# Kernel tuning notes

Hardware: AMD Instinct MI355X
Metric: run time of the kernel (lower is better)

Reference implementation:

```python
import jax, jax.numpy as jnp
import numpy as np

N, F, H, C = 50000, 128, 4, 32   # nodes, in_channels, heads, hidden_channels
E, R, DE = 800000, 8, 64         # edges, num_relations, edge_dim


def setup_inputs() -> dict:
    key = jax.random.key(0)
    ks = jax.random.split(key, 10)
    x = jax.random.normal(ks[0], (N, F), dtype=jnp.float32)
    edge_index = jax.random.randint(ks[1], (2, E), 0, N, dtype=jnp.int64)
    edge_type = jax.random.randint(ks[2], (E,), 0, R, dtype=jnp.int64)
    s_in = 1.0 / np.sqrt(F)
    s_e = 1.0 / np.sqrt(DE)
    edge_emb = jax.random.normal(ks[3], (R, DE), dtype=jnp.float32)
    Wq = jax.random.normal(ks[4], (F, H * C), dtype=jnp.float32) * s_in
    Wk = jax.random.normal(ks[5], (F, H * C), dtype=jnp.float32) * s_in
    Wv = jax.random.normal(ks[6], (F, H * C), dtype=jnp.float32) * s_in
    We = jax.random.normal(ks[7], (DE, H * C), dtype=jnp.float32) * s_e
    Wskip = jax.random.normal(ks[8], (F, H * C), dtype=jnp.float32) * s_in
    return {"x": x, "edge_index": edge_index, "edge_type": edge_type,
            "edge_emb": edge_emb, "Wq": Wq, "Wk": Wk, "Wv": Wv,
            "We": We, "Wskip": Wskip}


def reference(x, edge_index, edge_type, edge_emb, Wq, Wk, Wv, We, Wskip):
    # TransformerConv (PyG) with edge embeddings, concat heads, root skip, no bias.
    src, dst = edge_index[0], edge_index[1]
    q = (x @ Wq).reshape(N, H, C)
    k = (x @ Wk).reshape(N, H, C)
    v = (x @ Wv).reshape(N, H, C)
    e = (edge_emb[edge_type] @ We).reshape(E, H, C)      # per-edge relation emb
    kj = k[src] + e                                       # [E,H,C]
    logits = (q[dst] * kj).sum(-1) / jnp.sqrt(jnp.float32(C))  # [E,H]
    # segment softmax over incoming edges of each target node
    m = jax.ops.segment_max(logits, dst, num_segments=N)  # [N,H]
    m = jnp.where(jnp.isfinite(m), m, jnp.float32(0.0))
    ex = jnp.exp(logits - m[dst])
    denom = jax.ops.segment_sum(ex, dst, num_segments=N)  # [N,H]
    alpha = ex / (denom[dst] + 1e-16)                     # [E,H]
    msg = (v[src] + e) * alpha[:, :, None]                # [E,H,C]
    out = jax.ops.segment_sum(msg, dst, num_segments=N).reshape(N, H * C)
    return out + x @ Wskip
```

## Files before the change

kernel.cpp:

```cpp
#include <hip/hip_runtime.h>
#include <hip/hip_bf16.h>

#define NN 50000
#define FF 128
#define NH 4
#define CH 32
#define HC 128
#define NE 800000
#define NR 8
#define DEDIM 64
#define NBLK 196
#define PBLK 782
#define QKB 625
#define MTILES 3125

typedef __hip_bfloat16 bf16;
typedef __attribute__((ext_vector_type(8))) short short8;
typedef __attribute__((ext_vector_type(4))) float f32x4;

__device__ __forceinline__ float bflo(unsigned u) { return __uint_as_float(u << 16); }
__device__ __forceinline__ float bfhi(unsigned u) { return __uint_as_float(u & 0xFFFF0000u); }

__device__ __forceinline__ unsigned short f2bf(float f) {
  unsigned u = __float_as_uint(f);
  unsigned r = (u + 0x7FFFu + ((u >> 16) & 1u)) >> 16;
  return (unsigned short)r;
}
__device__ __forceinline__ unsigned pack2bf(float lo, float hi) {
  return (unsigned)f2bf(lo) | ((unsigned)f2bf(hi) << 16);
}

template <int ISBF>
__device__ __forceinline__ float ldf(const void* p, size_t i) {
  if (ISBF) return __bfloat162float(((const bf16*)p)[i]);
  return ((const float*)p)[i];
}

__global__ __launch_bounds__(256) void k_wt(const unsigned* __restrict__ xw,
    const void* __restrict__ Wq, const void* __restrict__ Ws,
    const void* __restrict__ Wk, const void* __restrict__ Wv,
    unsigned short* __restrict__ wtr) {
  unsigned ex = (xw[threadIdx.x & 63] >> 7) & 0xFFu;
  unsigned long long bb = __ballot(ex < 90u || ex > 140u);
  int isbf = (bb == 0ULL);
  int i = blockIdx.x * 256 + threadIdx.x;
  int m = i >> 14, n = (i >> 7) & 127, k = i & 127;
  const void* W = (m == 0) ? Wq : (m == 1) ? Ws : (m == 2) ? Wk : Wv;
  wtr[i] = isbf ? ((const unsigned short*)W)[k * HC + n]
                : f2bf(((const float*)W)[k * HC + n]);
}

__global__ __launch_bounds__(256) void k_prep(const unsigned* __restrict__ xw,
    const int* __restrict__ eidx32, const void* __restrict__ etype,
    const void* __restrict__ emb, const void* __restrict__ We,
    int* __restrict__ flag, int* __restrict__ hist, float* __restrict__ ee,
    unsigned* __restrict__ drk, int* __restrict__ setp) {
  __shared__ float es[NR * DEDIM];
  __shared__ int nzIdx, badBf;
  if (blockIdx.x < PBLK) {
    unsigned long long b = __ballot(eidx32[2 * (threadIdx.x & 63) + 1] != 0);
    int is64 = (b == 0ULL);
    int e0 = (blockIdx.x * 256 + threadIdx.x) * 4;
    if (e0 >= NE) return;
    int src[4], dst[4], et[4];
    if (is64) {
      const int4* p4 = (const int4*)eidx32;
      int4 a = p4[e0 >> 1],         b2 = p4[(e0 >> 1) + 1];
      int4 c = p4[(NE + e0) >> 1],  d  = p4[((NE + e0) >> 1) + 1];
      const int4* t4 = (const int4*)etype;
      int4 t0 = t4[e0 >> 1], t1 = t4[(e0 >> 1) + 1];
      src[0] = a.x; src[1] = a.z; src[2] = b2.x; src[3] = b2.z;
      dst[0] = c.x; dst[1] = c.z; dst[2] = d.x;  dst[3] = d.z;
      et[0] = t0.x; et[1] = t0.z; et[2] = t1.x;  et[3] = t1.z;
    } else {
      const int4* p4 = (const int4*)eidx32;
      int4 a = p4[e0 >> 2];
      int4 c = p4[(NE + e0) >> 2];
      const int4* t4 = (const int4*)etype;
      int4 t0 = t4[e0 >> 2];
      src[0] = a.x; src[1] = a.y; src[2] = a.z; src[3] = a.w;
      dst[0] = c.x; dst[1] = c.y; dst[2] = c.z; dst[3] = c.w;
      et[0] = t0.x; et[1] = t0.y; et[2] = t0.z; et[3] = t0.w;
    }
    unsigned dr[4]; int sp[4];
#pragma unroll
    for (int u = 0; u < 4; ++u) {
      int s  = min(max(src[u], 0), NN - 1);
      int dd = min(max(dst[u], 0), NN - 1);
      int tt = min(max(et[u], 0), NR - 1);
      int rank = atomicAdd(&hist[dd], 1);
      dr[u] = ((unsigned)dd << 16) | ((unsigned)rank & 0xFFFFu);
      sp[u] = (s << 3) | tt;
    }
    *(uint4*)&drk[e0]  = make_uint4(dr[0], dr[1], dr[2], dr[3]);
    *(int4*)&setp[e0]  = make_int4(sp[0], sp[1], sp[2], sp[3]);
    return;
  }
  if (threadIdx.x == 0) { nzIdx = 0; badBf = 0; }
  __syncthreads();
  if (threadIdx.x < 128) {
    if (eidx32[2 * threadIdx.x + 1] != 0) atomicAdd(&nzIdx, 1);
    unsigned e = (xw[threadIdx.x] >> 7) & 0xFFu;
    if (e < 90u || e > 140u) atomicAdd(&badBf, 1);
  }
  __syncthreads();
  const int isbf = (badBf == 0);
  if (threadIdx.x == 0) { flag[0] = (nzIdx == 0); flag[1] = isbf; }
  for (int i = threadIdx.x; i < NR * DEDIM; i += 256)
    es[i] = isbf ? ldf<1>(emb, i) : ldf<0>(emb, i);
  __syncthreads();
  for (int o = threadIdx.x; o < NR * HC; o += 256) {
    int r = o >> 7, j = o & 127;
    float acc = 0.f;
    if (isbf) { for (int d = 0; d < DEDIM; ++d) acc += es[r * DEDIM + d] * ldf<1>(We, d * HC + j); }
    else      { for (int d = 0; d < DEDIM; ++d) acc += es[r * DEDIM + d] * ldf<0>(We, d * HC + j); }
    ee[o] = acc;
  }
}

template <int ISBF>
__device__ __forceinline__ void qkvs4_body(const void* __restrict__ x,
    const unsigned short* __restrict__ wtr,
    unsigned short* __restrict__ qb, unsigned* __restrict__ kvb,
    void* __restrict__ out, unsigned char* __restrict__ est) {
  const int tid  = threadIdx.x;
  const int lane = tid & 63;
  const int wv   = tid >> 6;
  const int quad = lane >> 4;
  const int lr   = lane & 15;
  short8 bf[4][2][4];
#pragma unroll
  for (int m = 0; m < 4; ++m)
#pragma unroll
    for (int t = 0; t < 2; ++t) {
      int ncol = wv * 32 + t * 16 + lr;
#pragma unroll
      for (int kb = 0; kb < 4; ++kb)
        bf[m][t][kb] = *(const short8*)&wtr[(m * HC + ncol) * FF + kb * 32 + quad * 8];
    }
  unsigned short* qs  = (unsigned short*)est;
  unsigned short* sbs = (unsigned short*)(est + 4096);
  float*          sfs = (float*)(est + 4096);
  unsigned*       kvs = (unsigned*)est;
  const unsigned short* xu = (const unsigned short*)x;
  const float* xf = (const float*)x;
  const int mc = blockIdx.x;
  short8 lda[4];
  float4 raw[8];
  {
    size_t off = (size_t)(mc * 16 + lr) * FF + quad * 8;
    if (ISBF) {
#pragma unroll
      for (int kb = 0; kb < 4; ++kb) lda[kb] = *(const short8*)(xu + off + kb * 32);
    } else {
#pragma unroll
      for (int kb = 0; kb < 4; ++kb) {
        raw[2 * kb]     = *(const float4*)(xf + off + kb * 32);
        raw[2 * kb + 1] = *(const float4*)(xf + off + kb * 32 + 4);
      }
    }
  }
  for (int mt = mc; mt < MTILES; mt += QKB) {
    int m0 = mt * 16;
    short8 cur[4];
    if (ISBF) {
#pragma unroll
      for (int kb = 0; kb < 4; ++kb) cur[kb] = lda[kb];
    } else {
#pragma unroll
      for (int kb = 0; kb < 4; ++kb) {
        float4 a = raw[2 * kb], b = raw[2 * kb + 1];
        short8 o;
        o[0] = (short)f2bf(a.x); o[1] = (short)f2bf(a.y);
        o[2] = (short)f2bf(a.z); o[3] = (short)f2bf(a.w);
        o[4] = (short)f2bf(b.x); o[5] = (short)f2bf(b.y);
        o[6] = (short)f2bf(b.z); o[7] = (short)f2bf(b.w);
        cur[kb] = o;
      }
    }
    int mtn = mt + QKB;
    if (mtn < MTILES) {
      size_t off = (size_t)(mtn * 16 + lr) * FF + quad * 8;
      if (ISBF) {
#pragma unroll
        for (int kb = 0; kb < 4; ++kb) lda[kb] = *(const short8*)(xu + off + kb * 32);
      } else {
#pragma unroll
        for (int kb = 0; kb < 4; ++kb) {
          raw[2 * kb]     = *(const float4*)(xf + off + kb * 32);
          raw[2 * kb + 1] = *(const float4*)(xf + off + kb * 32 + 4);
        }
      }
    }
    f32x4 acc[4][2];
#pragma unroll
    for (int m = 0; m < 4; ++m)
#pragma unroll
      for (int t = 0; t < 2; ++t) acc[m][t] = {0.f, 0.f, 0.f, 0.f};
#pragma unroll
    for (int kb = 0; kb < 4; ++kb)
#pragma unroll
      for (int m = 0; m < 4; ++m) {
        acc[m][0] = __builtin_amdgcn_mfma_f32_16x16x32_bf16(cur[kb], bf[m][0][kb], acc[m][0], 0, 0, 0);
        acc[m][1] = __builtin_amdgcn_mfma_f32_16x16x32_bf16(cur[kb], bf[m][1][kb], acc[m][1], 0, 0, 0);
      }
#pragma unroll
    for (int t = 0; t < 2; ++t)
#pragma unroll
      for (int r = 0; r < 4; ++r) {
        int li = (quad * 4 + r) * HC + wv * 32 + t * 16 + lr;
        qs[li] = f2bf(acc[0][t][r]);
        if (ISBF) sbs[li] = f2bf(acc[1][t][r]);
        else      sfs[li] = acc[1][t][r];
      }
    __syncthreads();
    {
      int row = tid >> 4, seg = tid & 15;
      *(uint4*)(qb + (size_t)(m0 + row) * HC + seg * 8) = ((const uint4*)qs)[tid];
      if (ISBF) {
        *(uint4*)((unsigned short*)out + (size_t)(m0 + row) * HC + seg * 8) =
            ((const uint4*)sbs)[tid];
      } else {
#pragma unroll
        for (int s = 0; s < 2; ++s) {
          int idx = s * 256 + tid, rw = idx >> 5, sg = idx & 31;
          *(uint4*)((float*)out + (size_t)(m0 + rw) * HC + sg * 4) =
              ((const uint4*)sfs)[idx];
        }
      }
    }
    __syncthreads();
#pragma unroll
    for (int t = 0; t < 2; ++t)
#pragma unroll
      for (int r = 0; r < 4; ++r) {
        int li = (quad * 4 + r) * HC + wv * 32 + t * 16 + lr;
        kvs[li] = pack2bf(acc[2][t][r], acc[3][t][r]);
      }
    __syncthreads();
#pragma unroll
    for (int s = 0; s < 2; ++s) {
      int idx = s * 256 + tid, rw = idx >> 5, sg = idx & 31;
      *(uint4*)(kvb + (size_t)(m0 + rw) * HC + sg * 4) = ((const uint4*)kvs)[idx];
    }
    __syncthreads();
  }
}

__global__ __launch_bounds__(256, 2) void k_qkvs(const unsigned* __restrict__ xw,
    const unsigned short* __restrict__ wtr,
    unsigned short* __restrict__ qb, unsigned* __restrict__ kvb,
    void* __restrict__ out) {
  __shared__ __align__(16) unsigned char est[12288];
  unsigned ex = (xw[threadIdx.x & 63] >> 7) & 0xFFu;
  unsigned long long bb = __ballot(ex < 90u || ex > 140u);
  int isbf = (bb == 0ULL);
  if (isbf) qkvs4_body<1>(xw, wtr, qb, kvb, out, est);
  else      qkvs4_body<0>(xw, wtr, qb, kvb, out, est);
}

__global__ __launch_bounds__(256) void k_scan1(const int* __restrict__ hist,
                                               int* __restrict__ bsum) {
  __shared__ int red[4];
  int i = blockIdx.x * 256 + threadIdx.x;
  int v = (i < NN) ? hist[i] : 0;
#pragma unroll
  for (int m = 1; m < 64; m <<= 1) v += __shfl_xor(v, m);
  if ((threadIdx.x & 63) == 0) red[threadIdx.x >> 6] = v;
  __syncthreads();
  if (threadIdx.x == 0) bsum[blockIdx.x] = red[0] + red[1] + red[2] + red[3];
}

__global__ __launch_bounds__(256) void k_scan13(const int* __restrict__ hist,
    const int* __restrict__ bsum, int* __restrict__ rowptr) {
  __shared__ int s[256];
  int t = threadIdx.x;
  int bv = (t < NBLK) ? bsum[t] : 0;
  s[t] = bv;
  __syncthreads();
  for (int off = 1; off < 256; off <<= 1) {
    int u = (t >= off) ? s[t - off] : 0;
    __syncthreads();
    s[t] += u;
    __syncthreads();
  }
  int bexc = (blockIdx.x == 0) ? 0 : s[blockIdx.x - 1];
  __syncthreads();
  int i = blockIdx.x * 256 + t;
  int v = (i < NN) ? hist[i] : 0;
  s[t] = v;
  __syncthreads();
  for (int off = 1; off < 256; off <<= 1) {
    int u = (t >= off) ? s[t - off] : 0;
    __syncthreads();
    s[t] += u;
    __syncthreads();
  }
  int excl = bexc + s[t] - v;
  if (i < NN) rowptr[i] = excl;
  if (i == 0) rowptr[NN] = NE;
}

__global__ __launch_bounds__(256) void k_scatter(const unsigned* __restrict__ drk,
    const int* __restrict__ setp, const int* __restrict__ rowptr,
    int* __restrict__ srcet) {
  int e0 = (blockIdx.x * 256 + threadIdx.x) * 4;
  if (e0 >= NE) return;
  uint4 d4 = *(const uint4*)&drk[e0];
  int4  s4 = *(const int4*)&setp[e0];
  unsigned dd[4] = {d4.x, d4.y, d4.z, d4.w};
  int      sp[4] = {s4.x, s4.y, s4.z, s4.w};
#pragma unroll
  for (int u = 0; u < 4; ++u) {
    int pos = rowptr[dd[u] >> 16] + (int)(dd[u] & 0xFFFFu);
    pos = min(max(pos, 0), NE - 1);
    srcet[pos] = sp[u];
  }
}

__global__ __launch_bounds__(256) void k_gather(const int* __restrict__ rowptr,
    const int* __restrict__ srcet, const unsigned short* __restrict__ qb,
    const unsigned* __restrict__ kvb, const float* __restrict__ ee,
    const int* __restrict__ flag, void* __restrict__ out) {
  int n = blockIdx.x * 4 + (threadIdx.x >> 6);
  int l = threadIdx.x & 63;
  int t = l >> 5;
  int w = l & 31;
  int j0 = ((w >> 3) << 5) + ((w & 7) << 2);
  int beg = __builtin_amdgcn_readfirstlane(rowptr[n]);
  int end = __builtin_amdgcn_readfirstlane(rowptr[n + 1]);
  uint2 qw = *(const uint2*)(qb + (size_t)n * HC + j0);
  float q0 = bflo(qw.x), q1 = bfhi(qw.x), q2 = bflo(qw.y), q3 = bfhi(qw.y);
  const float sc = 0.17677669529663687f;
  float dn = 0.f, a0 = 0.f, a1 = 0.f, a2 = 0.f, a3 = 0.f;
  int p = beg;
  for (; p + 8 <= end; p += 8) {
    int se[4]; uint4 kv[4]; float4 ev[4];
#pragma unroll
    for (int u = 0; u < 4; ++u) se[u] = srcet[p + 2 * u + t];
#pragma unroll
    for (int u = 0; u < 4; ++u)
      kv[u] = *(const uint4*)(kvb + (size_t)(se[u] >> 3) * HC + j0);
#pragma unroll
    for (int u = 0; u < 4; ++u)
      ev[u] = *(const float4*)(ee + ((se[u] & 7) << 7) + j0);
#pragma unroll
    for (int u = 0; u < 4; ++u) {
      float pp = q0 * (bflo(kv[u].x) + ev[u].x) + q1 * (bflo(kv[u].y) + ev[u].y)
               + q2 * (bflo(kv[u].z) + ev[u].z) + q3 * (bflo(kv[u].w) + ev[u].w);
      pp += __shfl_xor(pp, 1);
      pp += __shfl_xor(pp, 2);
      pp += __shfl_xor(pp, 4);
      float xx = __expf(pp * sc);
      dn += xx;
      a0 += (bfhi(kv[u].x) + ev[u].x) * xx;
      a1 += (bfhi(kv[u].y) + ev[u].y) * xx;
      a2 += (bfhi(kv[u].z) + ev[u].z) * xx;
      a3 += (bfhi(kv[u].w) + ev[u].w) * xx;
    }
  }
  if (p < end) {
    int se[4]; bool ok[4]; uint4 kv[4]; float4 ev[4];
#pragma unroll
    for (int u = 0; u < 4; ++u) {
      int pe = p + 2 * u + t;
      ok[u] = pe < end;
      se[u] = srcet[ok[u] ? pe : beg];
    }
#pragma unroll
    for (int u = 0; u < 4; ++u)
      kv[u] = *(const uint4*)(kvb + (size_t)(se[u] >> 3) * HC + j0);
#pragma unroll
    for (int u = 0; u < 4; ++u)
      ev[u] = *(const float4*)(ee + ((se[u] & 7) << 7) + j0);
#pragma unroll
    for (int u = 0; u < 4; ++u) {
      float pp = q0 * (bflo(kv[u].x) + ev[u].x) + q1 * (bflo(kv[u].y) + ev[u].y)
               + q2 * (bflo(kv[u].z) + ev[u].z) + q3 * (bflo(kv[u].w) + ev[u].w);
      pp += __shfl_xor(pp, 1);
      pp += __shfl_xor(pp, 2);
      pp += __shfl_xor(pp, 4);
      float xx = ok[u] ? __expf(pp * sc) : 0.f;
      dn += xx;
      a0 += (bfhi(kv[u].x) + ev[u].x) * xx;
      a1 += (bfhi(kv[u].y) + ev[u].y) * xx;
      a2 += (bfhi(kv[u].z) + ev[u].z) * xx;
      a3 += (bfhi(kv[u].w) + ev[u].w) * xx;
    }
  }
  dn += __shfl_xor(dn, 32);
  a0 += __shfl_xor(a0, 32);
  a1 += __shfl_xor(a1, 32);
  a2 += __shfl_xor(a2, 32);
  a3 += __shfl_xor(a3, 32);
  if (t == 0) {
    float inv = 1.f / (dn + 1e-16f);
    size_t oi = (size_t)n * HC + j0;
    if (flag[1]) {
      uint2 sk = *(const uint2*)((const unsigned short*)out + oi);
      uint2 o;
      o.x = pack2bf(a0 * inv + bflo(sk.x), a1 * inv + bfhi(sk.x));
      o.y = pack2bf(a2 * inv + bflo(sk.y), a3 * inv + bfhi(sk.y));
      *(uint2*)((unsigned short*)out + oi) = o;
    } else {
      float4 sk = *(const float4*)((const float*)out + oi);
      float4 o = make_float4(a0 * inv + sk.x, a1 * inv + sk.y,
                             a2 * inv + sk.z, a3 * inv + sk.w);
      *(float4*)((float*)out + oi) = o;
    }
  }
}

extern "C" void kernel_launch(void* const* d_in, const int* in_sizes, int n_in,
                              void* d_out, int out_size, void* d_ws, size_t ws_size,
                              hipStream_t stream) {
  const void* x     = d_in[0];
  const void* eidx  = d_in[1];
  const void* etype = d_in[2];
  const void* emb   = d_in[3];
  const void* Wq    = d_in[4];
  const void* Wk    = d_in[5];
  const void* Wv    = d_in[6];
  const void* We    = d_in[7];
  const void* Ws    = d_in[8];

  float* base   = (float*)d_ws;
  int*   flag   = (int*)base;
  float* ee     = base + 16;
  int*   rowptr = (int*)(base + 1040);
  int*   bsum   = (int*)(base + 51044);
  unsigned short* wtr = (unsigned short*)(base + 51568);
  int*   srcet  = (int*)(base + 101568);
  int*   hist   = srcet;
  unsigned* drk = (unsigned*)(base + 901568);
  int*   setp   = (int*)(base + 1701568);
  unsigned short* qb  = (unsigned short*)(base + 2501568);
  unsigned*       kvb = (unsigned*)(base + 5701568);

  hipMemsetAsync(hist, 0, NN * sizeof(int), stream);
  k_wt     <<<256, 256, 0, stream>>>((const unsigned*)x, Wq, Ws, Wk, Wv, wtr);
  k_prep   <<<PBLK + 1, 256, 0, stream>>>((const unsigned*)x, (const int*)eidx,
                                          etype, emb, We, flag, hist, ee,
                                          drk, setp);
  k_qkvs   <<<QKB, 256, 0, stream>>>((const unsigned*)x, wtr, qb, kvb, d_out);
  k_scan1  <<<NBLK, 256, 0, stream>>>(hist, bsum);
  k_scan13 <<<NBLK, 256, 0, stream>>>(hist, bsum, rowptr);
  k_scatter<<<PBLK, 256, 0, stream>>>(drk, setp, rowptr, srcet);
  k_gather <<<NN / 4, 256, 0, stream>>>(rowptr, srcet, qb, kvb, ee, flag, d_out);
}
```

Baseline: 256.0 us.

## Fuse QKV projection and edge prep kernels; zero histogram inside weight transpose

Merges the QKV/skip projection kernel and the edge preprocessing kernel into one launch, with block ranges dispatched by block index. The histogram memset moves into the weight-transpose kernel. This removes a memset and one kernel launch, and lets the compute-bound GEMM blocks overlap with the atomic-heavy edge-prep blocks. The fused kernel loses the min-occupancy launch-bounds hint of the GEMM kernel, which may change register allocation.

```diff
diff --git a/kernel.cpp b/kernel.cpp
--- a/kernel.cpp
+++ b/kernel.cpp
@@ -39,7 +39,7 @@
 __global__ __launch_bounds__(256) void k_wt(const unsigned* __restrict__ xw,
     const void* __restrict__ Wq, const void* __restrict__ Ws,
     const void* __restrict__ Wk, const void* __restrict__ Wv,
-    unsigned short* __restrict__ wtr) {
+    unsigned short* __restrict__ wtr, int* __restrict__ hist) {
   unsigned ex = (xw[threadIdx.x & 63] >> 7) & 0xFFu;
   unsigned long long bb = __ballot(ex < 90u || ex > 140u);
   int isbf = (bb == 0ULL);
@@ -48,19 +48,159 @@
   const void* W = (m == 0) ? Wq : (m == 1) ? Ws : (m == 2) ? Wk : Wv;
   wtr[i] = isbf ? ((const unsigned short*)W)[k * HC + n]
                 : f2bf(((const float*)W)[k * HC + n]);
-}
-
-__global__ __launch_bounds__(256) void k_prep(const unsigned* __restrict__ xw,
+  if (i < NN) hist[i] = 0;
+}
+
+template <int ISBF>
+__device__ __forceinline__ void qkvs4_body(const void* __restrict__ x,
+    const unsigned short* __restrict__ wtr,
+    unsigned short* __restrict__ qb, unsigned* __restrict__ kvb,
+    void* __restrict__ out, unsigned char* __restrict__ est) {
+  const int tid  = threadIdx.x;
+  const int lane = tid & 63;
+  const int wv   = tid >> 6;
+  const int quad = lane >> 4;
+  const int lr   = lane & 15;
+  short8 bf[4][2][4];
+#pragma unroll
+  for (int m = 0; m < 4; ++m)
+#pragma unroll
+    for (int t = 0; t < 2; ++t) {
+      int ncol = wv * 32 + t * 16 + lr;
+#pragma unroll
+      for (int kb = 0; kb < 4; ++kb)
+        bf[m][t][kb] = *(const short8*)&wtr[(m * HC + ncol) * FF + kb * 32 + quad * 8];
+    }
+  unsigned short* qs  = (unsigned short*)est;
+  unsigned short* sbs = (unsigned short*)(est + 4096);
+  float*          sfs = (float*)(est + 4096);
+  unsigned*       kvs = (unsigned*)est;
+  const unsigned short* xu = (const unsigned short*)x;
+  const float* xf = (const float*)x;
+  const int mc = blockIdx.x;
+  short8 lda[4];
+  float4 raw[8];
+  {
+    size_t off = (size_t)(mc * 16 + lr) * FF + quad * 8;
+    if (ISBF) {
+#pragma unroll
+      for (int kb = 0; kb < 4; ++kb) lda[kb] = *(const short8*)(xu + off + kb * 32);
+    } else {
+#pragma unroll
+      for (int kb = 0; kb < 4; ++kb) {
+        raw[2 * kb]     = *(const float4*)(xf + off + kb * 32);
+        raw[2 * kb + 1] = *(const float4*)(xf + off + kb * 32 + 4);
+      }
+    }
+  }
+  for (int mt = mc; mt < MTILES; mt += QKB) {
+    int m0 = mt * 16;
+    short8 cur[4];
+    if (ISBF) {
+#pragma unroll
+      for (int kb = 0; kb < 4; ++kb) cur[kb] = lda[kb];
+    } else {
+#pragma unroll
+      for (int kb = 0; kb < 4; ++kb) {
+        float4 a = raw[2 * kb], b = raw[2 * kb + 1];
+        short8 o;
+        o[0] = (short)f2bf(a.x); o[1] = (short)f2bf(a.y);
+        o[2] = (short)f2bf(a.z); o[3] = (short)f2bf(a.w);
+        o[4] = (short)f2bf(b.x); o[5] = (short)f2bf(b.y);
+        o[6] = (short)f2bf(b.z); o[7] = (short)f2bf(b.w);
+        cur[kb] = o;
+      }
+    }
+    int mtn = mt + QKB;
+    if (mtn < MTILES) {
+      size_t off = (size_t)(mtn * 16 + lr) * FF + quad * 8;
+      if (ISBF) {
+#pragma unroll
+        for (int kb = 0; kb < 4; ++kb) lda[kb] = *(const short8*)(xu + off + kb * 32);
+      } else {
+#pragma unroll
+        for (int kb = 0; kb < 4; ++kb) {
+          raw[2 * kb]     = *(const float4*)(xf + off + kb * 32);
+          raw[2 * kb + 1] = *(const float4*)(xf + off + kb * 32 + 4);
+        }
+      }
+    }
+    f32x4 acc[4][2];
+#pragma unroll
+    for (int m = 0; m < 4; ++m)
+#pragma unroll
+      for (int t = 0; t < 2; ++t) acc[m][t] = {0.f, 0.f, 0.f, 0.f};
+#pragma unroll
+    for (int kb = 0; kb < 4; ++kb)
+#pragma unroll
+      for (int m = 0; m < 4; ++m) {
+        acc[m][0] = __builtin_amdgcn_mfma_f32_16x16x32_bf16(cur[kb], bf[m][0][kb], acc[m][0], 0, 0, 0);
+        acc[m][1] = __builtin_amdgcn_mfma_f32_16x16x32_bf16(cur[kb], bf[m][1][kb], acc[m][1], 0, 0, 0);
+      }
+#pragma unroll
+    for (int t = 0; t < 2; ++t)
+#pragma unroll
+      for (int r = 0; r < 4; ++r) {
+        int li = (quad * 4 + r) * HC + wv * 32 + t * 16 + lr;
+        qs[li] = f2bf(acc[0][t][r]);
+        if (ISBF) sbs[li] = f2bf(acc[1][t][r]);
+        else      sfs[li] = acc[1][t][r];
+      }
+    __syncthreads();
+    {
+      int row = tid >> 4, seg = tid & 15;
+      *(uint4*)(qb + (size_t)(m0 + row) * HC + seg * 8) = ((const uint4*)qs)[tid];
+      if (ISBF) {
+        *(uint4*)((unsigned short*)out + (size_t)(m0 + row) * HC + seg * 8) =
+            ((const uint4*)sbs)[tid];
+      } else {
+#pragma unroll
+        for (int s = 0; s < 2; ++s) {
+          int idx = s * 256 + tid, rw = idx >> 5, sg = idx & 31;
+          *(uint4*)((float*)out + (size_t)(m0 + rw) * HC + sg * 4) =
+              ((const uint4*)sfs)[idx];
+        }
+      }
+    }
+    __syncthreads();
+#pragma unroll
+    for (int t = 0; t < 2; ++t)
+#pragma unroll
+      for (int r = 0; r < 4; ++r) {
+        int li = (quad * 4 + r) * HC + wv * 32 + t * 16 + lr;
+        kvs[li] = pack2bf(acc[2][t][r], acc[3][t][r]);
+      }
+    __syncthreads();
+#pragma unroll
+    for (int s = 0; s < 2; ++s) {
+      int idx = s * 256 + tid, rw = idx >> 5, sg = idx & 31;
+      *(uint4*)(kvb + (size_t)(m0 + rw) * HC + sg * 4) = ((const uint4*)kvs)[idx];
+    }
+    __syncthreads();
+  }
+}
+
+__global__ __launch_bounds__(256) void k_fused(const unsigned* __restrict__ xw,
     const int* __restrict__ eidx32, const void* __restrict__ etype,
     const void* __restrict__ emb, const void* __restrict__ We,
+    const unsigned short* __restrict__ wtr,
     int* __restrict__ flag, int* __restrict__ hist, float* __restrict__ ee,
-    unsigned* __restrict__ drk, int* __restrict__ setp) {
-  __shared__ float es[NR * DEDIM];
-  __shared__ int nzIdx, badBf;
-  if (blockIdx.x < PBLK) {
+    unsigned* __restrict__ drk, int* __restrict__ setp,
+    unsigned short* __restrict__ qb, unsigned* __restrict__ kvb,
+    void* __restrict__ out) {
+  __shared__ __align__(16) unsigned char shm[12288];
+  if (blockIdx.x < QKB) {
+    unsigned ex = (xw[threadIdx.x & 63] >> 7) & 0xFFu;
+    unsigned long long bb = __ballot(ex < 90u || ex > 140u);
+    int isbf = (bb == 0ULL);
+    if (isbf) qkvs4_body<1>(xw, wtr, qb, kvb, out, shm);
+    else      qkvs4_body<0>(xw, wtr, qb, kvb, out, shm);
+    return;
+  }
+  if (blockIdx.x < QKB + PBLK) {
     unsigned long long b = __ballot(eidx32[2 * (threadIdx.x & 63) + 1] != 0);
     int is64 = (b == 0ULL);
-    int e0 = (blockIdx.x * 256 + threadIdx.x) * 4;
+    int e0 = ((blockIdx.x - QKB) * 256 + threadIdx.x) * 4;
     if (e0 >= NE) return;
     int src[4], dst[4], et[4];
     if (is64) {
@@ -96,6 +236,8 @@
     *(int4*)&setp[e0]  = make_int4(sp[0], sp[1], sp[2], sp[3]);
     return;
   }
+  float* es = (float*)shm;
+  __shared__ int nzIdx, badBf;
   if (threadIdx.x == 0) { nzIdx = 0; badBf = 0; }
   __syncthreads();
   if (threadIdx.x < 128) {
@@ -116,147 +258,6 @@
     else      { for (int d = 0; d < DEDIM; ++d) acc += es[r * DEDIM + d] * ldf<0>(We, d * HC + j); }
     ee[o] = acc;
   }
-}
-
-template <int ISBF>
-__device__ __forceinline__ void qkvs4_body(const void* __restrict__ x,
-    const unsigned short* __restrict__ wtr,
-    unsigned short* __restrict__ qb, unsigned* __restrict__ kvb,
-    void* __restrict__ out, unsigned char* __restrict__ est) {
-  const int tid  = threadIdx.x;
-  const int lane = tid & 63;
-  const int wv   = tid >> 6;
-  const int quad = lane >> 4;
-  const int lr   = lane & 15;
-  short8 bf[4][2][4];
-#pragma unroll
-  for (int m = 0; m < 4; ++m)
-#pragma unroll
-    for (int t = 0; t < 2; ++t) {
-      int ncol = wv * 32 + t * 16 + lr;
-#pragma unroll
-      for (int kb = 0; kb < 4; ++kb)
-        bf[m][t][kb] = *(const short8*)&wtr[(m * HC + ncol) * FF + kb * 32 + quad * 8];
-    }
-  unsigned short* qs  = (unsigned short*)est;
-  unsigned short* sbs = (unsigned short*)(est + 4096);
-  float*          sfs = (float*)(est + 4096);
-  unsigned*       kvs = (unsigned*)est;
-  const unsigned short* xu = (const unsigned short*)x;
-  const float* xf = (const float*)x;
-  const int mc = blockIdx.x;
-  short8 lda[4];
-  float4 raw[8];
-  {
-    size_t off = (size_t)(mc * 16 + lr) * FF + quad * 8;
-    if (ISBF) {
-#pragma unroll
-      for (int kb = 0; kb < 4; ++kb) lda[kb] = *(const short8*)(xu + off + kb * 32);
-    } else {
-#pragma unroll
-      for (int kb = 0; kb < 4; ++kb) {
-        raw[2 * kb]     = *(const float4*)(xf + off + kb * 32);
-        raw[2 * kb + 1] = *(const float4*)(xf + off + kb * 32 + 4);
-      }
-    }
-  }
-  for (int mt = mc; mt < MTILES; mt += QKB) {
-    int m0 = mt * 16;
-    short8 cur[4];
-    if (ISBF) {
-#pragma unroll
-      for (int kb = 0; kb < 4; ++kb) cur[kb] = lda[kb];
-    } else {
-#pragma unroll
-      for (int kb = 0; kb < 4; ++kb) {
-        float4 a = raw[2 * kb], b = raw[2 * kb + 1];
-        short8 o;
-        o[0] = (short)f2bf(a.x); o[1] = (short)f2bf(a.y);
-        o[2] = (short)f2bf(a.z); o[3] = (short)f2bf(a.w);
-        o[4] = (short)f2bf(b.x); o[5] = (short)f2bf(b.y);
-        o[6] = (short)f2bf(b.z); o[7] = (short)f2bf(b.w);
-        cur[kb] = o;
-      }
-    }
-    int mtn = mt + QKB;
-    if (mtn < MTILES) {
-      size_t off = (size_t)(mtn * 16 + lr) * FF + quad * 8;
-      if (ISBF) {
-#pragma unroll
-        for (int kb = 0; kb < 4; ++kb) lda[kb] = *(const short8*)(xu + off + kb * 32);
-      } else {
-#pragma unroll
-        for (int kb = 0; kb < 4; ++kb) {
-          raw[2 * kb]     = *(const float4*)(xf + off + kb * 32);
-          raw[2 * kb + 1] = *(const float4*)(xf + off + kb * 32 + 4);
-        }
-      }
-    }
-    f32x4 acc[4][2];
-#pragma unroll
-    for (int m = 0; m < 4; ++m)
-#pragma unroll
-      for (int t = 0; t < 2; ++t) acc[m][t] = {0.f, 0.f, 0.f, 0.f};
-#pragma unroll
-    for (int kb = 0; kb < 4; ++kb)
-#pragma unroll
-      for (int m = 0; m < 4; ++m) {
-        acc[m][0] = __builtin_amdgcn_mfma_f32_16x16x32_bf16(cur[kb], bf[m][0][kb], acc[m][0], 0, 0, 0);
-        acc[m][1] = __builtin_amdgcn_mfma_f32_16x16x32_bf16(cur[kb], bf[m][1][kb], acc[m][1], 0, 0, 0);
-      }
-#pragma unroll
-    for (int t = 0; t < 2; ++t)
-#pragma unroll
-      for (int r = 0; r < 4; ++r) {
-        int li = (quad * 4 + r) * HC + wv * 32 + t * 16 + lr;
-        qs[li] = f2bf(acc[0][t][r]);
-        if (ISBF) sbs[li] = f2bf(acc[1][t][r]);
-        else      sfs[li] = acc[1][t][r];
-      }
-    __syncthreads();
-    {
-      int row = tid >> 4, seg = tid & 15;
-      *(uint4*)(qb + (size_t)(m0 + row) * HC + seg * 8) = ((const uint4*)qs)[tid];
-      if (ISBF) {
-        *(uint4*)((unsigned short*)out + (size_t)(m0 + row) * HC + seg * 8) =
-            ((const uint4*)sbs)[tid];
-      } else {
-#pragma unroll
-        for (int s = 0; s < 2; ++s) {
-          int idx = s * 256 + tid, rw = idx >> 5, sg = idx & 31;
-          *(uint4*)((float*)out + (size_t)(m0 + rw) * HC + sg * 4) =
-              ((const uint4*)sfs)[idx];
-        }
-      }
-    }
-    __syncthreads();
-#pragma unroll
-    for (int t = 0; t < 2; ++t)
-#pragma unroll
-      for (int r = 0; r < 4; ++r) {
-        int li = (quad * 4 + r) * HC + wv * 32 + t * 16 + lr;
-        kvs[li] = pack2bf(acc[2][t][r], acc[3][t][r]);
-      }
-    __syncthreads();
-#pragma unroll
-    for (int s = 0; s < 2; ++s) {
-      int idx = s * 256 + tid, rw = idx >> 5, sg = idx & 31;
-      *(uint4*)(kvb + (size_t)(m0 + rw) * HC + sg * 4) = ((const uint4*)kvs)[idx];
-    }
-    __syncthreads();
-  }
-}
-
-__global__ __launch_bounds__(256, 2) void k_qkvs(const unsigned* __restrict__ xw,
-    const unsigned short* __restrict__ wtr,
-    unsigned short* __restrict__ qb, unsigned* __restrict__ kvb,
-    void* __restrict__ out) {
-  __shared__ __align__(16) unsigned char est[12288];
-  unsigned ex = (xw[threadIdx.x & 63] >> 7) & 0xFFu;
-  unsigned long long bb = __ballot(ex < 90u || ex > 140u);
-  int isbf = (bb == 0ULL);
-  if (isbf) qkvs4_body<1>(xw, wtr, qb, kvb, out, est);
-  else      qkvs4_body<0>(xw, wtr, qb, kvb, out, est);
 }
 
 __global__ __launch_bounds__(256) void k_scan1(const int* __restrict__ hist,
@@ -437,12 +438,12 @@
   unsigned short* qb  = (unsigned short*)(base + 2501568);
   unsigned*       kvb = (unsigned*)(base + 5701568);
 
-  hipMemsetAsync(hist, 0, NN * sizeof(int), stream);
-  k_wt     <<<256, 256, 0, stream>>>((const unsigned*)x, Wq, Ws, Wk, Wv, wtr);
-  k_prep   <<<PBLK + 1, 256, 0, stream>>>((const unsigned*)x, (const int*)eidx,
-                                          etype, emb, We, flag, hist, ee,
-                                          drk, setp);
-  k_qkvs   <<<QKB, 256, 0, stream>>>((const unsigned*)x, wtr, qb, kvb, d_out);
+  k_wt     <<<256, 256, 0, stream>>>((const unsigned*)x, Wq, Ws, Wk, Wv,
+                                     wtr, hist);
+  k_fused  <<<QKB + PBLK + 1, 256, 0, stream>>>((const unsigned*)x,
+                                                (const int*)eidx, etype, emb, We,
+                                                wtr, flag, hist, ee, drk, setp,
+                                                qb, kvb, d_out);
   k_scan1  <<<NBLK, 256, 0, stream>>>(hist, bsum);
   k_scan13 <<<NBLK, 256, 0, stream>>>(hist, bsum, rowptr);
   k_scatter<<<PBLK, 256, 0, stream>>>(drk, setp, rowptr, srcet);
```

New measurement: 258.9 us. Within noise of the previous version (+1.1%).
